# Performance work log

Hardware: AMD Instinct MI355X
Metric: run time of the kernel (lower is better)

## Reference

```python
import jax, jax.numpy as jnp
import numpy as np

N_NODES = 100_000   # number of nodes
N_EDGES = 1_600_000 # number of edges (avg degree 16)
D_IN    = 64        # node feature dim
E_W     = 16        # edge feature ('w') dim -> message dim D_IN + E_W
EPS     = 0.0       # init_eps, non-learnable buffer


def setup_inputs() -> dict:
    key = jax.random.key(0)
    k1, k2, k3, k4, k5 = jax.random.split(key, 5)
    feat = jax.random.normal(k1, (N_NODES, D_IN), dtype=jnp.float32)
    edge_w = jax.random.normal(k2, (N_EDGES, E_W), dtype=jnp.float32)
    src = jax.random.randint(k3, (N_EDGES,), 0, N_NODES)
    dst = jax.random.randint(k4, (N_EDGES,), 0, N_NODES)
    # apply_func: Linear(D_IN + E_W -> D_IN)
    W = jax.random.normal(k5, (D_IN + E_W, D_IN), dtype=jnp.float32) / np.float32(np.sqrt(D_IN + E_W))
    b = jnp.zeros((D_IN,), dtype=jnp.float32)
    return {"feat": feat, "edge_w": edge_w, "W": W, "b": b, "src": src, "dst": dst}


def reference(feat, edge_w, W, b, src, dst):
    n = feat.shape[0]
    # message m_e = concat(h[src_e], w_e); sum-aggregate over incoming edges of dst.
    # Sum of concat == concat of sums, avoiding materializing [E, D_IN+E_W].
    neigh_h = jax.ops.segment_sum(feat[src], dst, num_segments=n)     # [N, D_IN]
    neigh_w = jax.ops.segment_sum(edge_w, dst, num_segments=n)        # [N, E_W]
    neigh = jnp.concatenate([neigh_h, neigh_w], axis=-1)              # [N, D_IN+E_W]
    # pad feat with zeros to match widened message dim (as in the torch code)
    feat_pad = jnp.concatenate(
        [feat, jnp.zeros((n, neigh.shape[-1] - feat.shape[-1]), feat.dtype)], axis=-1
    )
    rst = (1.0 + EPS) * feat_pad + neigh                              # eps-residual
    rst = rst @ W + b                                                 # apply_func (Linear)
    return jax.nn.relu(rst)                                           # activation
```

## Files before the change

### kernel.cpp

```cpp
#include <hip/hip_runtime.h>

#define D_IN  64
#define E_W   16
#define D_MSG 80
#define NXCD  8

static __device__ __forceinline__ void f4add(float4& a, const float4& b) {
    a.x += b.x; a.y += b.y; a.z += b.z; a.w += b.w;
}

__global__ __launch_bounds__(256) void k_hist_sh(const int4* __restrict__ dst4,
                                                 const int* __restrict__ dst,
                                                 int* __restrict__ deg,
                                                 int E, int rng)
{
    int shard = blockIdx.x & (NXCD - 1);
    int wg    = blockIdx.x / NXCD;
    int lo    = shard * rng;
    int hi    = lo + rng;
    int E4    = E >> 2;

    int base = wg * 512;
    int stop = min(base + 512, E4);
    for (int i = base + threadIdx.x; i < stop; i += 256) {
        int4 d = dst4[i];
        if (d.x >= lo && d.x < hi) atomicAdd(deg + d.x, 1);
        if (d.y >= lo && d.y < hi) atomicAdd(deg + d.y, 1);
        if (d.z >= lo && d.z < hi) atomicAdd(deg + d.z, 1);
        if (d.w >= lo && d.w < hi) atomicAdd(deg + d.w, 1);
    }
    if (wg == 0 && threadIdx.x < (E & 3)) {
        int e = (E & ~3) + threadIdx.x;
        int d = dst[e];
        if (d >= lo && d < hi) atomicAdd(deg + d, 1);
    }
}

__global__ __launch_bounds__(256) void k_scan1(const int* __restrict__ deg,
                                               int* __restrict__ excl,
                                               int* __restrict__ bsums, int n)
{
    __shared__ int ts[256];
    int base = blockIdx.x * 1024 + threadIdx.x * 4;
    int v[4], s = 0;
    #pragma unroll
    for (int i = 0; i < 4; ++i) { v[i] = (base + i < n) ? deg[base + i] : 0; s += v[i]; }
    ts[threadIdx.x] = s; __syncthreads();
    #pragma unroll
    for (int off = 1; off < 256; off <<= 1) {
        int t = (threadIdx.x >= off) ? ts[threadIdx.x - off] : 0;
        __syncthreads();
        ts[threadIdx.x] += t;
        __syncthreads();
    }
    int run = ts[threadIdx.x] - s;
    if (threadIdx.x == 255) bsums[blockIdx.x] = ts[255];
    #pragma unroll
    for (int i = 0; i < 4; ++i) {
        if (base + i < n) excl[base + i] = run;
        run += v[i];
    }
}

__global__ __launch_bounds__(256) void k_scan2(int* __restrict__ bsums,
                                               int* __restrict__ bexcl, int nb)
{
    __shared__ int ts[256];
    int v = (threadIdx.x < nb) ? bsums[threadIdx.x] : 0;
    ts[threadIdx.x] = v; __syncthreads();
    #pragma unroll
    for (int off = 1; off < 256; off <<= 1) {
        int t = (threadIdx.x >= off) ? ts[threadIdx.x - off] : 0;
        __syncthreads();
        ts[threadIdx.x] += t;
        __syncthreads();
    }
    bexcl[threadIdx.x] = ts[threadIdx.x] - v;
}

__global__ __launch_bounds__(256) void k_scan3(const int* __restrict__ excl,
                                               const int* __restrict__ bexcl,
                                               int* __restrict__ offsets,
                                               int* __restrict__ cursor, int n, int E)
{
    int i = blockIdx.x * 256 + threadIdx.x;
    if (i < n) {
        int s = excl[i] + bexcl[i >> 10];
        offsets[i] = s;
        cursor[i]  = s;
    }
    if (i == 0) offsets[n] = E;
}

__global__ __launch_bounds__(256) void k_reorder_sh(const int4* __restrict__ src4,
                                                    const int4* __restrict__ dst4,
                                                    const int* __restrict__ src,
                                                    const int* __restrict__ dst,
                                                    int* __restrict__ cursor,
                                                    int2* __restrict__ sorted,
                                                    int E, int rng)
{
    int shard = blockIdx.x & (NXCD - 1);
    int wg    = blockIdx.x / NXCD;
    int lo    = shard * rng;
    int hi    = lo + rng;
    int E4    = E >> 2;

    int base = wg * 512;
    int stop = min(base + 512, E4);
    for (int i = base + threadIdx.x; i < stop; i += 256) {
        int4 d = dst4[i];
        bool any = (d.x >= lo && d.x < hi) | (d.y >= lo && d.y < hi) |
                   (d.z >= lo && d.z < hi) | (d.w >= lo && d.w < hi);
        if (!any) continue;
        int4 s = src4[i];
        int e = i * 4;
        if (d.x >= lo && d.x < hi) sorted[atomicAdd(cursor + d.x, 1)] = make_int2(s.x, e + 0);
        if (d.y >= lo && d.y < hi) sorted[atomicAdd(cursor + d.y, 1)] = make_int2(s.y, e + 1);
        if (d.z >= lo && d.z < hi) sorted[atomicAdd(cursor + d.z, 1)] = make_int2(s.z, e + 2);
        if (d.w >= lo && d.w < hi) sorted[atomicAdd(cursor + d.w, 1)] = make_int2(s.w, e + 3);
    }
    if (wg == 0 && threadIdx.x < (E & 3)) {
        int e = (E & ~3) + threadIdx.x;
        int d = dst[e];
        if (d >= lo && d < hi) sorted[atomicAdd(cursor + d, 1)] = make_int2(src[e], e);
    }
}

__global__ __launch_bounds__(256) void k_pull(const float4* __restrict__ feat4,
                                              const float4* __restrict__ ew4,
                                              const int2* __restrict__ sorted,
                                              const int* __restrict__ offsets,
                                              float4* __restrict__ acc_h4,
                                              float4* __restrict__ acc_w4, int N)
{
    int t = blockIdx.x * 256 + threadIdx.x;
    int node = t >> 4;
    if (node >= N) return;
    int l = t & 15;

    int beg = offsets[node];
    int end = offsets[node + 1];

    float4 ah = feat4[(size_t)node * 16 + l];
    float4 aw = make_float4(0.f, 0.f, 0.f, 0.f);

    if (beg < end) {
        int2 r0 = sorted[beg];
        int2 r1 = (beg + 1 < end) ? sorted[beg + 1] : make_int2(0, 0);
        for (int p = beg; p < end; ++p) {
            int2 rn = (p + 2 < end) ? sorted[p + 2] : make_int2(0, 0);
            float4 h0 = feat4[(size_t)r0.x * 16 + l];
            f4add(ah, h0);
            if (l < 4) {
                float4 w0 = ew4[(size_t)r0.y * 4 + l];
                f4add(aw, w0);
            }
            r0 = r1; r1 = rn;
        }
    }

    acc_h4[(size_t)node * 16 + l] = ah;
    if (l < 4) acc_w4[(size_t)node * 4 + l] = aw;
}

__global__ __launch_bounds__(256) void scatter_kernel(
    const float4* __restrict__ feat4, const float4* __restrict__ ew4,
    const int* __restrict__ src, const int* __restrict__ dst,
    float* __restrict__ acc_h, float* __restrict__ acc_w, int E)
{
    int t = blockIdx.x * 256 + threadIdx.x;
    int e = t >> 4;
    if (e >= E) return;
    int l = t & 15;
    int s = src[e];
    int d = dst[e];
    float4 hv = feat4[(size_t)s * 16 + l];
    float4 wv;
    bool do_w = (l < 4);
    if (do_w) wv = ew4[(size_t)e * 4 + l];
    float* p = acc_h + (size_t)d * D_IN + l * 4;
    unsafeAtomicAdd(p + 0, hv.x);
    unsafeAtomicAdd(p + 1, hv.y);
    unsafeAtomicAdd(p + 2, hv.z);
    unsafeAtomicAdd(p + 3, hv.w);
    if (do_w) {
        float* q = acc_w + (size_t)d * E_W + l * 4;
        unsafeAtomicAdd(q + 0, wv.x);
        unsafeAtomicAdd(q + 1, wv.y);
        unsafeAtomicAdd(q + 2, wv.z);
        unsafeAtomicAdd(q + 3, wv.w);
    }
}

__global__ __launch_bounds__(256) void gemm_relu_kernel(
    const float* __restrict__ feat, const float* __restrict__ acc_w,
    const float* __restrict__ Wm, const float* __restrict__ bias,
    float* __restrict__ out, int N, int add_feat)
{
    __shared__ float4 Wl[D_MSG * 16];
    __shared__ float4 bl4[16];
    __shared__ float  xs[64 * 84];

    for (int i = threadIdx.x; i < D_MSG * 16; i += 256)
        Wl[i] = ((const float4*)Wm)[i];
    if (threadIdx.x < 16)
        bl4[threadIdx.x] = ((const float4*)bias)[threadIdx.x];

    const int tc   = threadIdx.x & 15;
    const int tg   = threadIdx.x >> 4;
    const int base = blockIdx.x * 64;

    for (int i = threadIdx.x; i < 64 * 20; i += 256) {
        int r = i / 20, c = i % 20;
        int row = base + r;
        float4 v = make_float4(0.f, 0.f, 0.f, 0.f);
        if (row < N) {
            if (c < 16) {
                v = ((const float4*)out)[(size_t)row * 16 + c];
                if (add_feat) {
                    float4 f = ((const float4*)feat)[(size_t)row * 16 + c];
                    f4add(v, f);
                }
            } else {
                v = ((const float4*)acc_w)[(size_t)row * 4 + (c - 16)];
            }
        }
        *((float4*)&xs[r * 84 + c * 4]) = v;
    }
    __syncthreads();

    float4 ob = bl4[tc];
    float4 acc[4];
    acc[0] = ob; acc[1] = ob; acc[2] = ob; acc[3] = ob;

    #pragma unroll 4
    for (int k = 0; k < D_MSG; ++k) {
        float4 w = Wl[k * 16 + tc];
        #pragma unroll
        for (int rr = 0; rr < 4; ++rr) {
            float xk = xs[(tg * 4 + rr) * 84 + k];
            acc[rr].x += xk * w.x;
            acc[rr].y += xk * w.y;
            acc[rr].z += xk * w.z;
            acc[rr].w += xk * w.w;
        }
    }

    #pragma unroll
    for (int rr = 0; rr < 4; ++rr) {
        int row = base + tg * 4 + rr;
        if (row < N) {
            float4 v = acc[rr];
            v.x = fmaxf(v.x, 0.f);
            v.y = fmaxf(v.y, 0.f);
            v.z = fmaxf(v.z, 0.f);
            v.w = fmaxf(v.w, 0.f);
            ((float4*)out)[(size_t)row * 16 + tc] = v;
        }
    }
}

static inline size_t align256(size_t x) { return (x + 255) & ~(size_t)255; }

extern "C" void kernel_launch(void* const* d_in, const int* in_sizes, int n_in,
                              void* d_out, int out_size, void* d_ws, size_t ws_size,
                              hipStream_t stream) {
    const float* feat   = (const float*)d_in[0];
    const float* edge_w = (const float*)d_in[1];
    const float* Wm     = (const float*)d_in[2];
    const float* bias   = (const float*)d_in[3];
    const int*   src    = (const int*)d_in[4];
    const int*   dst    = (const int*)d_in[5];
    float* out = (float*)d_out;

    const int N = in_sizes[0] / D_IN;
    const int E = in_sizes[4];

    size_t o_accw   = 0;
    size_t o_deg    = align256(o_accw + (size_t)N * E_W * 4);
    size_t o_excl   = align256(o_deg  + (size_t)(N + 1) * 4);
    size_t o_off    = align256(o_excl + (size_t)N * 4);
    size_t o_cur    = align256(o_off  + (size_t)(N + 1) * 4);
    size_t o_bsum   = align256(o_cur  + (size_t)N * 4);
    size_t o_bexcl  = align256(o_bsum + 256 * 4);
    size_t o_sorted = align256(o_bexcl + 256 * 4);
    size_t need     = o_sorted + (size_t)E * 8;

    char* ws = (char*)d_ws;
    float* acc_w = (float*)(ws + o_accw);

    int used_fallback = 0;

    if (ws_size >= need) {
        int*  deg     = (int*) (ws + o_deg);
        int*  excl    = (int*) (ws + o_excl);
        int*  offsets = (int*) (ws + o_off);
        int*  cursor  = (int*) (ws + o_cur);
        int*  bsums   = (int*) (ws + o_bsum);
        int*  bexcl   = (int*) (ws + o_bexcl);
        int2* sorted  = (int2*)(ws + o_sorted);

        hipMemsetAsync(deg, 0, (size_t)(N + 1) * 4, stream);

        const int rng = (N + NXCD - 1) / NXCD;
        const int E4  = E >> 2;
        const int wg_per_shard = (E4 + 511) / 512;
        const int grid_sh = wg_per_shard * NXCD;

        k_hist_sh<<<grid_sh, 256, 0, stream>>>(
            (const int4*)dst, dst, deg, E, rng);

        int nb1 = (N + 1023) / 1024;
        k_scan1<<<nb1, 256, 0, stream>>>(deg, excl, bsums, N);
        k_scan2<<<1, 256, 0, stream>>>(bsums, bexcl, nb1);
        k_scan3<<<(N + 255) / 256, 256, 0, stream>>>(excl, bexcl, offsets, cursor, N, E);

        k_reorder_sh<<<grid_sh, 256, 0, stream>>>(
            (const int4*)src, (const int4*)dst, src, dst, cursor, sorted, E, rng);

        k_pull<<<(N * 16 + 255) / 256, 256, 0, stream>>>(
            (const float4*)feat, (const float4*)edge_w, sorted, offsets,
            (float4*)out, (float4*)acc_w, N);
    } else {
        used_fallback = 1;
        hipMemsetAsync(d_out, 0, (size_t)N * D_IN * sizeof(float), stream);
        hipMemsetAsync(acc_w, 0, (size_t)N * E_W * sizeof(float), stream);
        long long tot = (long long)E * 16;
        scatter_kernel<<<(int)((tot + 255) / 256), 256, 0, stream>>>(
            (const float4*)feat, (const float4*)edge_w, src, dst, out, acc_w, E);
    }

    gemm_relu_kernel<<<(N + 63) / 64, 256, 0, stream>>>(
        feat, acc_w, Wm, bias, out, N, used_fallback);
}
```

Before: 419.8 us.

## Permute edge features into CSR order during reorder for sequential pull reads

The reorder kernel now writes both the source index and the full 64-byte edge feature row into dst-sorted order, so the pull kernel reads edge features sequentially instead of gathering them by edge id. This removes random 64-byte gathers from the pull phase. In exchange, the reorder step moves an extra E*64 bytes through scattered writes and needs a much larger workspace. When the workspace is too small, the code falls back to the old path.

```diff
diff --git a/kernel.cpp b/kernel.cpp
--- a/kernel.cpp
+++ b/kernel.cpp
@@ -90,6 +90,101 @@
         cursor[i]  = s;
     }
     if (i == 0) offsets[n] = E;
+}
+
+__global__ __launch_bounds__(256) void k_reorder_ew(const int4* __restrict__ src4,
+                                                    const int4* __restrict__ dst4,
+                                                    const int* __restrict__ src,
+                                                    const int* __restrict__ dst,
+                                                    const float4* __restrict__ ew4,
+                                                    int* __restrict__ cursor,
+                                                    int* __restrict__ ssrc,
+                                                    float4* __restrict__ sew4,
+                                                    int E, int rng)
+{
+    int shard = blockIdx.x & (NXCD - 1);
+    int wg    = blockIdx.x / NXCD;
+    int lo    = shard * rng;
+    int hi    = lo + rng;
+    int E4    = E >> 2;
+
+    int base = wg * 512;
+    int stop = min(base + 512, E4);
+    for (int i = base + threadIdx.x; i < stop; i += 256) {
+        int4 d = dst4[i];
+        bool h0 = (d.x >= lo && d.x < hi), h1 = (d.y >= lo && d.y < hi);
+        bool h2 = (d.z >= lo && d.z < hi), h3 = (d.w >= lo && d.w < hi);
+        if (!(h0 | h1 | h2 | h3)) continue;
+        int4 s = src4[i];
+        int e = i * 4;
+        if (h0) {
+            int pos = atomicAdd(cursor + d.x, 1); ssrc[pos] = s.x;
+            const float4* sp = ew4 + (size_t)(e + 0) * 4;
+            float4* dp = sew4 + (size_t)pos * 4;
+            dp[0] = sp[0]; dp[1] = sp[1]; dp[2] = sp[2]; dp[3] = sp[3];
+        }
+        if (h1) {
+            int pos = atomicAdd(cursor + d.y, 1); ssrc[pos] = s.y;
+            const float4* sp = ew4 + (size_t)(e + 1) * 4;
+            float4* dp = sew4 + (size_t)pos * 4;
+            dp[0] = sp[0]; dp[1] = sp[1]; dp[2] = sp[2]; dp[3] = sp[3];
+        }
+        if (h2) {
+            int pos = atomicAdd(cursor + d.z, 1); ssrc[pos] = s.z;
+            const float4* sp = ew4 + (size_t)(e + 2) * 4;
+            float4* dp = sew4 + (size_t)pos * 4;
+            dp[0] = sp[0]; dp[1] = sp[1]; dp[2] = sp[2]; dp[3] = sp[3];
+        }
+        if (h3) {
+            int pos = atomicAdd(cursor + d.w, 1); ssrc[pos] = s.w;
+            const float4* sp = ew4 + (size_t)(e + 3) * 4;
+            float4* dp = sew4 + (size_t)pos * 4;
+            dp[0] = sp[0]; dp[1] = sp[1]; dp[2] = sp[2]; dp[3] = sp[3];
+        }
+    }
+    if (wg == 0 && threadIdx.x < (E & 3)) {
+        int e = (E & ~3) + threadIdx.x;
+        int d = dst[e];
+        if (d >= lo && d < hi) {
+            int pos = atomicAdd(cursor + d, 1); ssrc[pos] = src[e];
+            const float4* sp = ew4 + (size_t)e * 4;
+            float4* dp = sew4 + (size_t)pos * 4;
+            dp[0] = sp[0]; dp[1] = sp[1]; dp[2] = sp[2]; dp[3] = sp[3];
+        }
+    }
+}
+
+__global__ __launch_bounds__(256) void k_pull_seq(const float4* __restrict__ feat4,
+                                                  const float4* __restrict__ sew4,
+                                                  const int* __restrict__ ssrc,
+                                                  const int* __restrict__ offsets,
+                                                  float4* __restrict__ acc_h4,
+                                                  float4* __restrict__ acc_w4, int N)
+{
+    int t = blockIdx.x * 256 + threadIdx.x;
+    int node = t >> 4;
+    if (node >= N) return;
+    int l = t & 15;
+
+    int beg = offsets[node];
+    int end = offsets[node + 1];
+
+    float4 ah = feat4[(size_t)node * 16 + l];
+    float4 aw = make_float4(0.f, 0.f, 0.f, 0.f);
+
+    if (beg < end) {
+        int s0 = ssrc[beg];
+        int s1 = (beg + 1 < end) ? ssrc[beg + 1] : 0;
+        for (int p = beg; p < end; ++p) {
+            int sn = (p + 2 < end) ? ssrc[p + 2] : 0;
+            f4add(ah, feat4[(size_t)s0 * 16 + l]);
+            if (l < 4) f4add(aw, sew4[(size_t)p * 4 + l]);
+            s0 = s1; s1 = sn;
+        }
+    }
+
+    acc_h4[(size_t)node * 16 + l] = ah;
+    if (l < 4) acc_w4[(size_t)node * 4 + l] = aw;
 }
 
 __global__ __launch_bounds__(256) void k_reorder_sh(const int4* __restrict__ src4,
@@ -150,12 +245,8 @@
         int2 r1 = (beg + 1 < end) ? sorted[beg + 1] : make_int2(0, 0);
         for (int p = beg; p < end; ++p) {
             int2 rn = (p + 2 < end) ? sorted[p + 2] : make_int2(0, 0);
-            float4 h0 = feat4[(size_t)r0.x * 16 + l];
-            f4add(ah, h0);
-            if (l < 4) {
-                float4 w0 = ew4[(size_t)r0.y * 4 + l];
-                f4add(aw, w0);
-            }
+            f4add(ah, feat4[(size_t)r0.x * 16 + l]);
+            if (l < 4) f4add(aw, ew4[(size_t)r0.y * 4 + l]);
             r0 = r1; r1 = rn;
         }
     }
@@ -284,22 +375,25 @@
     size_t o_cur    = align256(o_off  + (size_t)(N + 1) * 4);
     size_t o_bsum   = align256(o_cur  + (size_t)N * 4);
     size_t o_bexcl  = align256(o_bsum + 256 * 4);
-    size_t o_sorted = align256(o_bexcl + 256 * 4);
-    size_t need     = o_sorted + (size_t)E * 8;
+    size_t o_tail   = align256(o_bexcl + 256 * 4);
+    size_t o_ssrc   = o_tail;
+    size_t o_sew    = align256(o_ssrc + (size_t)E * 4);
+    size_t need_full = o_sew + (size_t)E * 64;
+    size_t o_sorted = o_tail;
+    size_t need_mid = o_sorted + (size_t)E * 8;
 
     char* ws = (char*)d_ws;
     float* acc_w = (float*)(ws + o_accw);
 
     int used_fallback = 0;
 
-    if (ws_size >= need) {
-        int*  deg     = (int*) (ws + o_deg);
-        int*  excl    = (int*) (ws + o_excl);
-        int*  offsets = (int*) (ws + o_off);
-        int*  cursor  = (int*) (ws + o_cur);
-        int*  bsums   = (int*) (ws + o_bsum);
-        int*  bexcl   = (int*) (ws + o_bexcl);
-        int2* sorted  = (int2*)(ws + o_sorted);
+    if (ws_size >= need_mid) {
+        int* deg     = (int*)(ws + o_deg);
+        int* excl    = (int*)(ws + o_excl);
+        int* offsets = (int*)(ws + o_off);
+        int* cursor  = (int*)(ws + o_cur);
+        int* bsums   = (int*)(ws + o_bsum);
+        int* bexcl   = (int*)(ws + o_bexcl);
 
         hipMemsetAsync(deg, 0, (size_t)(N + 1) * 4, stream);
 
@@ -308,20 +402,30 @@
         const int wg_per_shard = (E4 + 511) / 512;
         const int grid_sh = wg_per_shard * NXCD;
 
-        k_hist_sh<<<grid_sh, 256, 0, stream>>>(
-            (const int4*)dst, dst, deg, E, rng);
+        k_hist_sh<<<grid_sh, 256, 0, stream>>>((const int4*)dst, dst, deg, E, rng);
 
         int nb1 = (N + 1023) / 1024;
         k_scan1<<<nb1, 256, 0, stream>>>(deg, excl, bsums, N);
         k_scan2<<<1, 256, 0, stream>>>(bsums, bexcl, nb1);
         k_scan3<<<(N + 255) / 256, 256, 0, stream>>>(excl, bexcl, offsets, cursor, N, E);
 
-        k_reorder_sh<<<grid_sh, 256, 0, stream>>>(
-            (const int4*)src, (const int4*)dst, src, dst, cursor, sorted, E, rng);
-
-        k_pull<<<(N * 16 + 255) / 256, 256, 0, stream>>>(
-            (const float4*)feat, (const float4*)edge_w, sorted, offsets,
-            (float4*)out, (float4*)acc_w, N);
+        if (ws_size >= need_full) {
+            int*    ssrc = (int*)   (ws + o_ssrc);
+            float4* sew4 = (float4*)(ws + o_sew);
+            k_reorder_ew<<<grid_sh, 256, 0, stream>>>(
+                (const int4*)src, (const int4*)dst, src, dst,
+                (const float4*)edge_w, cursor, ssrc, sew4, E, rng);
+            k_pull_seq<<<(N * 16 + 255) / 256, 256, 0, stream>>>(
+                (const float4*)feat, sew4, ssrc, offsets,
+                (float4*)out, (float4*)acc_w, N);
+        } else {
+            int2* sorted = (int2*)(ws + o_sorted);
+            k_reorder_sh<<<grid_sh, 256, 0, stream>>>(
+                (const int4*)src, (const int4*)dst, src, dst, cursor, sorted, E, rng);
+            k_pull<<<(N * 16 + 255) / 256, 256, 0, stream>>>(
+                (const float4*)feat, (const float4*)edge_w, sorted, offsets,
+                (float4*)out, (float4*)acc_w, N);
+        }
     } else {
         used_fallback = 1;
         hipMemsetAsync(d_out, 0, (size_t)N * D_IN * sizeof(float), stream);
```

Result: slower. 518.7 us (+23.5%).
